# Performance work log

Hardware: AMD Instinct MI355X
Metric: run time of the kernel (lower is better)

Reference implementation:

```python
import jax, jax.numpy as jnp
import numpy as np

B, S, E, H, A, V, T = 64, 128, 512, 512, 256, 8192, 32


def setup_inputs() -> dict:
    key = jax.random.key(0)
    ks = jax.random.split(key, 10)
    sc = 0.02
    b_lstm = jnp.zeros((4 * H,), jnp.float32).at[H:2 * H].set(1.0)  # forget-gate bias = 1
    return {
        "encoder_features": jax.random.normal(ks[0], (B, S, E), jnp.float32),
        "target_sequence": jax.random.randint(ks[1], (B, T), 0, V),
        "emb": jax.random.uniform(ks[2], (V, H), jnp.float32, -0.1, 0.1),
        "W_enc": jax.random.normal(ks[3], (E, A), jnp.float32) * sc,
        "W_dec": jax.random.normal(ks[4], (H, A), jnp.float32) * sc,
        "b_att": jnp.zeros((A,), jnp.float32),
        "v_att": jax.random.normal(ks[5], (A,), jnp.float32) * sc,
        "W_ih": jax.random.normal(ks[6], (4 * H, H + E), jnp.float32) * sc,
        "W_hh": jax.random.normal(ks[7], (4 * H, H), jnp.float32) * sc,
        "b_ih": b_lstm,
        "b_hh": jnp.zeros((4 * H,), jnp.float32),
        "W_out": jax.random.normal(ks[8], (V, H + E), jnp.float32) * sc,
        "b_out": jnp.zeros((V,), jnp.float32),
    }


def reference(encoder_features, target_sequence, emb, W_enc, W_dec, b_att, v_att,
              W_ih, W_hh, b_ih, b_hh, W_out, b_out):
    b, t = target_sequence.shape
    # teacher forcing: first input token is 0, then shifted targets -> [T, B]
    tokens = jnp.concatenate(
        [jnp.zeros((b, 1), target_sequence.dtype), target_sequence[:, :-1]], axis=1).T
    # precompute encoder projection of Bahdanau attention: [B, S, A]
    enc_proj = jnp.einsum('bse,ea->bsa', encoder_features, W_enc)
    bias = b_ih + b_hh
    h0 = jnp.zeros((b, H), encoder_features.dtype)
    c0 = jnp.zeros((b, H), encoder_features.dtype)

    def step(carry, tok):
        h, c = carry
        x_emb = jnp.take(emb, tok, axis=0)                      # [B, H]
        # Bahdanau attention using previous decoder hidden state h
        e = jnp.tanh(enc_proj + (h @ W_dec + b_att)[:, None, :])  # [B, S, A]
        scores = jnp.einsum('bsa,a->bs', e, v_att)               # [B, S]
        w = jax.nn.softmax(scores, axis=-1)
        ctx = jnp.einsum('bs,bse->be', w, encoder_features)      # [B, E]
        x = jnp.concatenate([x_emb, ctx], axis=-1)               # [B, H+E]
        gates = x @ W_ih.T + h @ W_hh.T + bias                   # [B, 4H]
        i, f, g, o = jnp.split(gates, 4, axis=-1)
        c_new = jax.nn.sigmoid(f) * c + jax.nn.sigmoid(i) * jnp.tanh(g)
        h_new = jax.nn.sigmoid(o) * jnp.tanh(c_new)
        out = jnp.concatenate([h_new, ctx], axis=-1) @ W_out.T + b_out  # [B, V]
        return (h_new, c_new), out

    _, outs = jax.lax.scan(step, (h0, c0), tokens)
    return outs.transpose(1, 0, 2)  # [B, T, V]
```

## Files before the change

### kernel.cpp

```cpp
#include <hip/hip_runtime.h>
#include <math.h>

#define BB 64
#define SS 128
#define EE 512
#define HH 512
#define AA 256
#define VV 8192
#define TT 32

typedef __bf16 bf16x8 __attribute__((ext_vector_type(8)));
typedef __bf16 bf16x4 __attribute__((ext_vector_type(4)));
typedef float  f32x4  __attribute__((ext_vector_type(4)));

__device__ __forceinline__ bf16x8 cvt_v(float4 u, float4 v) {
    bf16x8 r;
    r[0] = (__bf16)u.x; r[1] = (__bf16)u.y; r[2] = (__bf16)u.z; r[3] = (__bf16)u.w;
    r[4] = (__bf16)v.x; r[5] = (__bf16)v.y; r[6] = (__bf16)v.z; r[7] = (__bf16)v.w;
    return r;
}

__device__ __forceinline__ float tanh_fast(float x) {
    x = fminf(15.f, fmaxf(-15.f, x));
    float e = __expf(2.f * x);
    return (e - 1.f) / (e + 1.f);
}
__device__ __forceinline__ float sigmoid_fast(float x) {
    return 1.f / (1.f + __expf(-x));
}

#define LDW(d, p) { const float4* q_ = (const float4*)(p); d##0 = q_[0]; d##1 = q_[1]; d##2 = q_[2]; d##3 = q_[3]; }

__global__ __launch_bounds__(256) void gemm_nn(
    const float* __restrict__ A, int lda,
    const float* __restrict__ B, int ldb,
    float* __restrict__ C, int ldc, int K)
{
    __shared__ float As[16][68];
    __shared__ float Bs[16][68];
    const int tid = threadIdx.x;
    const int m0 = blockIdx.x * 64, n0 = blockIdx.y * 64;
    const int row = tid >> 2, kq = (tid & 3) * 4;
    const int kk = tid >> 4, nq = (tid & 15) * 4;
    const int tm = tid >> 4, tn = tid & 15;
    float acc[4][4] = {};
    for (int k0 = 0; k0 < K; k0 += 16) {
        float4 av = *(const float4*)(A + (size_t)(m0 + row) * lda + k0 + kq);
        float4 bv = *(const float4*)(B + (size_t)(k0 + kk) * ldb + n0 + nq);
        As[kq + 0][row] = av.x; As[kq + 1][row] = av.y;
        As[kq + 2][row] = av.z; As[kq + 3][row] = av.w;
        *(float4*)&Bs[kk][nq] = bv;
        __syncthreads();
#pragma unroll
        for (int k = 0; k < 16; ++k) {
            float4 a = *(const float4*)&As[k][tm * 4];
            float4 b = *(const float4*)&Bs[k][tn * 4];
            acc[0][0] += a.x * b.x; acc[0][1] += a.x * b.y; acc[0][2] += a.x * b.z; acc[0][3] += a.x * b.w;
            acc[1][0] += a.y * b.x; acc[1][1] += a.y * b.y; acc[1][2] += a.y * b.z; acc[1][3] += a.y * b.w;
            acc[2][0] += a.z * b.x; acc[2][1] += a.z * b.y; acc[2][2] += a.z * b.z; acc[2][3] += a.z * b.w;
            acc[3][0] += a.w * b.x; acc[3][1] += a.w * b.y; acc[3][2] += a.w * b.z; acc[3][3] += a.w * b.w;
        }
        __syncthreads();
    }
#pragma unroll
    for (int i = 0; i < 4; ++i) {
        float4 r = make_float4(acc[i][0], acc[i][1], acc[i][2], acc[i][3]);
        *(float4*)(C + (size_t)(m0 + tm * 4 + i) * ldc + n0 + tn * 4) = r;
    }
}

__global__ __launch_bounds__(256) void k_cvt_bf16(
    const float* __restrict__ src, __bf16* __restrict__ dst, size_t n4)
{
    size_t i = (size_t)blockIdx.x * 256 + threadIdx.x;
    if (i < n4) {
        float4 v = *(const float4*)(src + i * 4);
        bf16x4 r;
        r[0] = (__bf16)v.x; r[1] = (__bf16)v.y; r[2] = (__bf16)v.z; r[3] = (__bf16)v.w;
        *(bf16x4*)(dst + i * 4) = r;
    }
}

__global__ __launch_bounds__(256) void k_cvt_gates(
    const float* __restrict__ W_ih, const float* __restrict__ W_hh,
    __bf16* __restrict__ Wg)
{
    const int n = blockIdx.x;
    const int j = ((n & 3) << 9) + (n >> 2);
    for (int k = threadIdx.x * 4; k < 1536; k += 1024) {
        const float* src = (k < 512)  ? (W_hh + (size_t)j * 512 + k)
                         : (k < 1024) ? (W_ih + (size_t)j * 1024 + k)
                                      : (W_ih + (size_t)j * 1024 + (k - 1024));
        float4 v = *(const float4*)src;
        bf16x4 r;
        r[0] = (__bf16)v.x; r[1] = (__bf16)v.y; r[2] = (__bf16)v.z; r[3] = (__bf16)v.w;
        *(bf16x4*)(Wg + (size_t)n * 1536 + k) = r;
    }
}

__global__ __launch_bounds__(1024) void attn_step(
    const float* __restrict__ encf,
    const float* __restrict__ encp,
    const float* __restrict__ W_dec,
    const float* __restrict__ b_att,
    const float* __restrict__ v_att,
    const float* __restrict__ emb,
    const int*   __restrict__ tgt,
    const float* __restrict__ h,
    __bf16* __restrict__ xh_cur,
    __bf16* __restrict__ XHN,
    int t)
{
    const int b = blockIdx.x;
    const int tid = threadIdx.x;
    __shared__ float sh[512];
    __shared__ float sdec[256];
    __shared__ float sv[256];
    __shared__ float sw[128], st[128];
    __shared__ float part[4][256];
    __shared__ float cpart[2][512];

    if (tid < 512) sh[tid] = h[(size_t)b * 512 + tid];
    else if (tid < 768) sv[tid - 512] = v_att[tid - 512];
    __syncthreads();

    {
        const int a = tid & 255, kq = tid >> 8;
        const float* w = W_dec + (size_t)kq * 128 * 256 + a;
        const float* hp = sh + kq * 128;
        float s = 0.f;
#pragma unroll 8
        for (int k = 0; k < 128; ++k) s += hp[k] * w[(size_t)k * 256];
        part[kq][a] = s;
    }
    __syncthreads();
    if (tid < 256)
        sdec[tid] = part[0][tid] + part[1][tid] + part[2][tid] + part[3][tid] + b_att[tid];
    __syncthreads();

    {
        const int wv = tid >> 6, lane = tid & 63;
#pragma unroll
        for (int i = 0; i < 8; ++i) {
            const int s = wv * 8 + i;
            const float* ep = encp + ((size_t)b * 128 + s) * 256;
            float sum = 0.f;
#pragma unroll
            for (int c = 0; c < 4; ++c) {
                int a = lane + 64 * c;
                sum += tanh_fast(ep[a] + sdec[a]) * sv[a];
            }
#pragma unroll
            for (int off = 32; off > 0; off >>= 1) sum += __shfl_down(sum, off);
            if (lane == 0) sw[s] = sum;
        }
    }
    __syncthreads();

    if (tid < 128) st[tid] = sw[tid];
    __syncthreads();
    for (int off = 64; off > 0; off >>= 1) {
        if (tid < off) st[tid] = fmaxf(st[tid], st[tid + off]);
        __syncthreads();
    }
    const float mx = st[0];
    __syncthreads();
    if (tid < 128) { float ex = __expf(sw[tid] - mx); sw[tid] = ex; st[tid] = ex; }
    __syncthreads();
    for (int off = 64; off > 0; off >>= 1) {
        if (tid < off) st[tid] += st[tid + off];
        __syncthreads();
    }

    {
        const int e = tid & 511, half = tid >> 9;
        const float* ef = encf + (size_t)b * (SS * EE) + (size_t)half * 64 * 512 + e;
        const float* wp = sw + half * 64;
        float cv = 0.f;
#pragma unroll 8
        for (int s = 0; s < 64; ++s) cv += wp[s] * ef[(size_t)s * 512];
        cpart[half][e] = cv;
    }
    __syncthreads();
    const float inv = 1.f / st[0];
    if (tid < 512) {
        const __bf16 cv = (__bf16)((cpart[0][tid] + cpart[1][tid]) * inv);
        xh_cur[(size_t)b * 1024 + tid] = cv;
        XHN[(size_t)(t * 64 + b) * 1024 + 512 + tid] = cv;
    } else {
        const int e = tid - 512;
        const int tok = (t == 0) ? 0 : tgt[b * TT + t - 1];
        xh_cur[(size_t)b * 1024 + 512 + e] = (__bf16)emb[(size_t)tok * 512 + e];
    }
}

template<bool BF16W>
__global__ __launch_bounds__(256) void gemm_gates_lstm(
    const __bf16* __restrict__ h_old,
    const __bf16* __restrict__ xh_ce,
    const float* __restrict__ W_ih, const float* __restrict__ W_hh,
    const __bf16* __restrict__ Wg,
    const float* __restrict__ b_ih, const float* __restrict__ b_hh,
    float* __restrict__ hbuf, float* __restrict__ cbuf,
    __bf16* __restrict__ h_new,
    __bf16* __restrict__ XHN, int t)
{
    __shared__ __align__(16) char smem[18432];
    __bf16 (*Ws)[32][72] = (__bf16 (*)[32][72])smem;
    float  (*Cf)[36]     = (float (*)[36])(smem + 9216);
    const int tid = threadIdx.x;
    const int wv = tid >> 6, lane = tid & 63;
    const int quad = lane >> 4, l16 = lane & 15;
    const int n0 = blockIdx.x * 32;
    const int rowW = tid >> 3, kq8 = (tid & 7) * 8;

    const __bf16* rB = nullptr;
    const float *rH = nullptr, *rI = nullptr;
    if constexpr (BF16W) {
        rB = Wg + (size_t)(n0 + rowW) * 1536 + kq8;
    } else {
        const int nglob = n0 + rowW;
        const int j = ((nglob & 3) << 9) + (nglob >> 2);
        rH = W_hh + (size_t)j * 512;
        rI = W_ih + (size_t)j * 1024;
    }
    auto wld = [&](int it) -> bf16x8 {
        if constexpr (BF16W) {
            return *(const bf16x8*)(rB + it * 64);
        } else {
            const int k = it * 64 + kq8;
            const float* s = (k < 512) ? (rH + k)
                           : (k < 1024 ? rI + k : rI + (k - 1024));
            const float4* q = (const float4*)s;
            return cvt_v(q[0], q[1]);
        }
    };
    const __bf16* aHp = h_old + (size_t)(wv * 16 + l16) * 512 + quad * 8;
    const __bf16* aXp = xh_ce + (size_t)(wv * 16 + l16) * 1024 + quad * 8;

    f32x4 acc[2] = {{0,0,0,0},{0,0,0,0}};
    bf16x8 wcur = wld(0), wnxt = wld(1);
    bf16x8 aC0 = *(const bf16x8*)aHp, aC1 = *(const bf16x8*)(aHp + 32);
    bf16x8 aN0, aN1;
    for (int it = 0; it < 24; ++it) {
        *(bf16x8*)&Ws[it & 1][rowW][kq8] = wcur;
        __syncthreads();
        wcur = wnxt;
        if (it + 2 < 24) wnxt = wld(it + 2);
        if (it + 1 < 24) {
            const int itn = it + 1;
            const __bf16* ap = (itn < 8) ? (aHp + itn * 64) : (aXp + (itn - 8) * 64);
            aN0 = *(const bf16x8*)ap; aN1 = *(const bf16x8*)(ap + 32);
        }
#pragma unroll
        for (int c = 0; c < 2; ++c) {
            bf16x8 b0 = *(const bf16x8*)&Ws[it & 1][c * 16 + l16][quad * 8];
            bf16x8 b1 = *(const bf16x8*)&Ws[it & 1][c * 16 + l16][quad * 8 + 32];
            acc[c] = __builtin_amdgcn_mfma_f32_16x16x32_bf16(aC0, b0, acc[c], 0, 0, 0);
            acc[c] = __builtin_amdgcn_mfma_f32_16x16x32_bf16(aC1, b1, acc[c], 0, 0, 0);
        }
        aC0 = aN0; aC1 = aN1;
    }
    __syncthreads();
#pragma unroll
    for (int r = 0; r < 4; ++r) {
        Cf[wv * 16 + quad * 4 + r][ 0 + l16] = acc[0][r];
        Cf[wv * 16 + quad * 4 + r][16 + l16] = acc[1][r];
    }
    __syncthreads();
    const int U0 = n0 >> 2;
#pragma unroll
    for (int pass = 0; pass < 2; ++pass) {
        const int it2 = tid + pass * 256;
        const int bb = it2 >> 3, ul = it2 & 7;
        const int u = U0 + ul;
        const float gi = Cf[bb][4 * ul + 0] + b_ih[u]          + b_hh[u];
        const float gf = Cf[bb][4 * ul + 1] + b_ih[512 + u]    + b_hh[512 + u];
        const float gg = Cf[bb][4 * ul + 2] + b_ih[1024 + u]   + b_hh[1024 + u];
        const float go = Cf[bb][4 * ul + 3] + b_ih[1536 + u]   + b_hh[1536 + u];
        const float si = sigmoid_fast(gi);
        const float sf = sigmoid_fast(gf);
        const float so = sigmoid_fast(go);
        const float cn = sf * cbuf[bb * 512 + u] + si * tanh_fast(gg);
        const float hn = so * tanh_fast(cn);
        cbuf[bb * 512 + u] = cn;
        hbuf[bb * 512 + u] = hn;
        const __bf16 hb = (__bf16)hn;
        h_new[(size_t)bb * 512 + u] = hb;
        if (XHN) XHN[(size_t)(t * 64 + bb) * 1024 + u] = hb;
    }
}

template<bool BF16W>
__global__ __launch_bounds__(256) void gemm_out_big(
    const __bf16* __restrict__ XHN,
    const float*  __restrict__ Wo_f,
    const __bf16* __restrict__ Wo_b,
    const float*  __restrict__ b_out,
    float* __restrict__ out)
{
    __shared__ __bf16 Bs[2][64][72];
    const int tid = threadIdx.x;
    const int blk = blockIdx.x;
    const int mt = blk & 15;
    const int n0 = (blk >> 4) * 64;
    const int wv = tid >> 6, lane = tid & 63;
    const int quad = lane >> 4, l16 = lane & 15;
    const int row = tid >> 2, cq = tid & 3;

    const __bf16* aP0 = XHN + (size_t)(mt * 128 + wv * 16 + l16) * 1024 + quad * 8;
    const __bf16* aP1 = aP0 + (size_t)64 * 1024;

    f32x4 acc[8] = {{0,0,0,0},{0,0,0,0},{0,0,0,0},{0,0,0,0},
                    {0,0,0,0},{0,0,0,0},{0,0,0,0},{0,0,0,0}};
    float4 wA0, wA1, wA2, wA3, wB0, wB1, wB2, wB3;
    bf16x8 pA0, pA1, pB0, pB1;
    const float*  bsf = nullptr;
    const __bf16* bsb = nullptr;
    if constexpr (BF16W) {
        bsb = Wo_b + (size_t)(n0 + row) * 1024 + cq * 16;
        const bf16x8* q0 = (const bf16x8*)bsb;        pA0 = q0[0]; pA1 = q0[1];
        const bf16x8* q1 = (const bf16x8*)(bsb + 64); pB0 = q1[0]; pB1 = q1[1];
    } else {
        bsf = Wo_f + (size_t)(n0 + row) * 1024 + cq * 16;
        LDW(wA, bsf); LDW(wB, bsf + 64);
    }
    bf16x8 a0C0 = *(const bf16x8*)aP0, a0C1 = *(const bf16x8*)(aP0 + 32);
    bf16x8 a1C0 = *(const bf16x8*)aP1, a1C1 = *(const bf16x8*)(aP1 + 32);
    bf16x8 a0N0, a0N1, a1N0, a1N1;

    for (int it = 0; it < 16; ++it) {
        __bf16* dst = &Bs[it & 1][row][cq * 16];
        if constexpr (BF16W) {
            *(bf16x8*)dst       = pA0;
            *(bf16x8*)(dst + 8) = pA1;
        } else {
            *(bf16x8*)dst       = cvt_v(wA0, wA1);
            *(bf16x8*)(dst + 8) = cvt_v(wA2, wA3);
        }
        __syncthreads();
        if constexpr (BF16W) {
            pA0 = pB0; pA1 = pB1;
            if (it + 2 < 16) {
                const bf16x8* q = (const bf16x8*)(bsb + (it + 2) * 64);
                pB0 = q[0]; pB1 = q[1];
            }
        } else {
            wA0 = wB0; wA1 = wB1; wA2 = wB2; wA3 = wB3;
            if (it + 2 < 16) LDW(wB, bsf + (it + 2) * 64);
        }
        if (it + 1 < 16) {
            const __bf16* ap0 = aP0 + (it + 1) * 64;
            const __bf16* ap1 = aP1 + (it + 1) * 64;
            a0N0 = *(const bf16x8*)ap0; a0N1 = *(const bf16x8*)(ap0 + 32);
            a1N0 = *(const bf16x8*)ap1; a1N1 = *(const bf16x8*)(ap1 + 32);
        }
#pragma unroll
        for (int c = 0; c < 4; ++c) {
            bf16x8 b0 = *(const bf16x8*)&Bs[it & 1][c * 16 + l16][quad * 8];
            bf16x8 b1 = *(const bf16x8*)&Bs[it & 1][c * 16 + l16][quad * 8 + 32];
            acc[c]     = __builtin_amdgcn_mfma_f32_16x16x32_bf16(a0C0, b0, acc[c],     0, 0, 0);
            acc[c]     = __builtin_amdgcn_mfma_f32_16x16x32_bf16(a0C1, b1, acc[c],     0, 0, 0);
            acc[4 + c] = __builtin_amdgcn_mfma_f32_16x16x32_bf16(a1C0, b0, acc[4 + c], 0, 0, 0);
            acc[4 + c] = __builtin_amdgcn_mfma_f32_16x16x32_bf16(a1C1, b1, acc[4 + c], 0, 0, 0);
        }
        a0C0 = a0N0; a0C1 = a0N1; a1C0 = a1N0; a1C1 = a1N1;
    }
    const int nb = n0 + l16;
#pragma unroll
    for (int h2 = 0; h2 < 2; ++h2) {
#pragma unroll
        for (int r = 0; r < 4; ++r) {
            const int rglob = mt * 128 + h2 * 64 + wv * 16 + quad * 4 + r;
            const int tstep = rglob >> 6, bb = rglob & 63;
            float* orow = out + (size_t)bb * (TT * VV) + (size_t)tstep * VV + nb;
            orow[ 0] = acc[h2 * 4 + 0][r] + b_out[nb +  0];
            orow[16] = acc[h2 * 4 + 1][r] + b_out[nb + 16];
            orow[32] = acc[h2 * 4 + 2][r] + b_out[nb + 32];
            orow[48] = acc[h2 * 4 + 3][r] + b_out[nb + 48];
        }
    }
}

template<bool BF16W>
__global__ __launch_bounds__(256) void fused_out_attn(
    const __bf16* __restrict__ hA, const __bf16* __restrict__ xA,
    const float*  __restrict__ Wo_f, const __bf16* __restrict__ Wo_b,
    const float*  __restrict__ b_out, float* __restrict__ out, int tprev,
    const float* __restrict__ encf, const float* __restrict__ encp,
    const float* __restrict__ W_dec, const float* __restrict__ b_att,
    const float* __restrict__ v_att, const float* __restrict__ emb,
    const int*   __restrict__ tgt, const float* __restrict__ h,
    __bf16* __restrict__ xh_cur, int t, int nOut)
{
    __shared__ __align__(16) char smem[18432];
    const int blk = blockIdx.x;
    const int tid = threadIdx.x;
    const int wv = tid >> 6, lane = tid & 63;
    const int quad = lane >> 4, l16 = lane & 15;

    if (blk < nOut) {
        __bf16 (*Bs)[64][72] = (__bf16 (*)[64][72])smem;
        const int n0 = blk * 64;
        const int row = tid >> 2, cq = tid & 3;
        const __bf16* aHp = hA + (size_t)(wv * 16 + l16) * 512 + quad * 8;
        const __bf16* aXp = xA + (size_t)(wv * 16 + l16) * 1024 + quad * 8;

        f32x4 acc[4] = {{0,0,0,0},{0,0,0,0},{0,0,0,0},{0,0,0,0}};
        bf16x8 aC0 = *(const bf16x8*)aHp, aC1 = *(const bf16x8*)(aHp + 32);
        bf16x8 aN0, aN1;
        float4 wA0, wA1, wA2, wA3, wB0, wB1, wB2, wB3;
        bf16x8 pA0, pA1, pB0, pB1;
        const float*  bsf = nullptr;
        const __bf16* bsb = nullptr;
        if constexpr (BF16W) {
            bsb = Wo_b + (size_t)(n0 + row) * 1024 + cq * 16;
            const bf16x8* q0 = (const bf16x8*)bsb;        pA0 = q0[0]; pA1 = q0[1];
            const bf16x8* q1 = (const bf16x8*)(bsb + 64); pB0 = q1[0]; pB1 = q1[1];
        } else {
            bsf = Wo_f + (size_t)(n0 + row) * 1024 + cq * 16;
            LDW(wA, bsf); LDW(wB, bsf + 64);
        }
        for (int it = 0; it < 16; ++it) {
            __bf16* dst = &Bs[it & 1][row][cq * 16];
            if constexpr (BF16W) {
                *(bf16x8*)dst       = pA0;
                *(bf16x8*)(dst + 8) = pA1;
            } else {
                *(bf16x8*)dst       = cvt_v(wA0, wA1);
                *(bf16x8*)(dst + 8) = cvt_v(wA2, wA3);
            }
            __syncthreads();
            if constexpr (BF16W) {
                pA0 = pB0; pA1 = pB1;
                if (it + 2 < 16) {
                    const bf16x8* q = (const bf16x8*)(bsb + (it + 2) * 64);
                    pB0 = q[0]; pB1 = q[1];
                }
            } else {
                wA0 = wB0; wA1 = wB1; wA2 = wB2; wA3 = wB3;
                if (it + 2 < 16) LDW(wB, bsf + (it + 2) * 64);
            }
            if (it + 1 < 16) {
                const int itn = it + 1;
                const __bf16* ap = (itn < 8) ? (aHp + itn * 64) : (aXp + (itn - 8) * 64);
                aN0 = *(const bf16x8*)ap; aN1 = *(const bf16x8*)(ap + 32);
            }
#pragma unroll
            for (int c = 0; c < 4; ++c) {
                bf16x8 b0 = *(const bf16x8*)&Bs[it & 1][c * 16 + l16][quad * 8];
                bf16x8 b1 = *(const bf16x8*)&Bs[it & 1][c * 16 + l16][quad * 8 + 32];
                acc[c] = __builtin_amdgcn_mfma_f32_16x16x32_bf16(aC0, b0, acc[c], 0, 0, 0);
                acc[c] = __builtin_amdgcn_mfma_f32_16x16x32_bf16(aC1, b1, acc[c], 0, 0, 0);
            }
            aC0 = aN0; aC1 = aN1;
        }
        const int m = wv * 16 + quad * 4;
        const int nb = n0 + l16;
        float* op = out + (size_t)tprev * VV + nb;
#pragma unroll
        for (int r = 0; r < 4; ++r) {
            float* orow = op + (size_t)(m + r) * (TT * VV);
            orow[ 0] = acc[0][r] + b_out[nb +  0];
            orow[16] = acc[1][r] + b_out[nb + 16];
            orow[32] = acc[2][r] + b_out[nb + 32];
            orow[48] = acc[3][r] + b_out[nb + 48];
        }
    } else {
        const int b = blk - nOut;
        float* sh   = (float*)smem;
        float* sdec = sh + 512;
        float* sv   = sdec + 256;
        float* sw   = sv + 256;
        sh[tid] = h[(size_t)b * 512 + tid];
        sh[tid + 256] = h[(size_t)b * 512 + 256 + tid];
        sv[tid] = v_att[tid];
        __syncthreads();
        {
            const float* w = W_dec + tid;
            float s = 0.f;
#pragma unroll 8
            for (int k = 0; k < 512; ++k) s += sh[k] * w[(size_t)k * 256];
            sdec[tid] = s + b_att[tid];
        }
        __syncthreads();
        {
            const float* ep0 = encp + ((size_t)b * 128 + wv * 32) * 256;
            for (int i = 0; i < 32; ++i) {
                const float* ep = ep0 + (size_t)i * 256;
                float sum = 0.f;
#pragma unroll
                for (int c = 0; c < 4; ++c) {
                    int a = lane + 64 * c;
                    sum += tanh_fast(ep[a] + sdec[a]) * sv[a];
                }
#pragma unroll
                for (int off = 32; off > 0; off >>= 1) sum += __shfl_down(sum, off);
                if (lane == 0) sw[wv * 32 + i] = sum;
            }
        }
        __syncthreads();
        if (tid < 64) {
            float a0 = sw[tid], a1 = sw[tid + 64];
            float m = fmaxf(a0, a1);
#pragma unroll
            for (int off = 32; off > 0; off >>= 1) m = fmaxf(m, __shfl_xor(m, off));
            float e0 = __expf(a0 - m), e1 = __expf(a1 - m);
            sw[tid] = e0; sw[tid + 64] = e1;
            float ss = e0 + e1;
#pragma unroll
            for (int off = 32; off > 0; off >>= 1) ss += __shfl_xor(ss, off);
            if (tid == 0) sh[0] = ss;
        }
        __syncthreads();
        const float inv = 1.f / sh[0];
        {
            const float* ef = encf + (size_t)b * (SS * EE) + tid;
            float cv0 = 0.f, cv1 = 0.f;
#pragma unroll 8
            for (int s = 0; s < 128; ++s) {
                float w = sw[s];
                cv0 += w * ef[(size_t)s * 512];
                cv1 += w * ef[(size_t)s * 512 + 256];
            }
            xh_cur[(size_t)b * 1024 + tid]       = (__bf16)(cv0 * inv);
            xh_cur[(size_t)b * 1024 + 256 + tid] = (__bf16)(cv1 * inv);
        }
        {
            const int tok = (t == 0) ? 0 : tgt[b * TT + t - 1];
            const float* em = emb + (size_t)tok * 512;
            xh_cur[(size_t)b * 1024 + 512 + tid] = (__bf16)em[tid];
            xh_cur[(size_t)b * 1024 + 768 + tid] = (__bf16)em[tid + 256];
        }
    }
}

__global__ void k_zero_f(float* p, int n) {
    int i = blockIdx.x * 256 + threadIdx.x;
    if (i < n) p[i] = 0.f;
}
__global__ void k_zero_bf(__bf16* p, int n) {
    int i = blockIdx.x * 256 + threadIdx.x;
    if (i < n) p[i] = (__bf16)0.f;
}

extern "C" void kernel_launch(void* const* d_in, const int* in_sizes, int n_in,
                              void* d_out, int out_size, void* d_ws, size_t ws_size,
                              hipStream_t stream)
{
    (void)in_sizes; (void)n_in; (void)out_size;
    const float* encf  = (const float*)d_in[0];
    const int*   tgt   = (const int*)  d_in[1];
    const float* emb   = (const float*)d_in[2];
    const float* W_enc = (const float*)d_in[3];
    const float* W_dec = (const float*)d_in[4];
    const float* b_att = (const float*)d_in[5];
    const float* v_att = (const float*)d_in[6];
    const float* W_ih  = (const float*)d_in[7];
    const float* W_hh  = (const float*)d_in[8];
    const float* b_ih  = (const float*)d_in[9];
    const float* b_hh  = (const float*)d_in[10];
    const float* W_out = (const float*)d_in[11];
    const float* b_out = (const float*)d_in[12];
    float* out = (float*)d_out;

    float* ws = (float*)d_ws;
    size_t off = 0;
    auto alloc = [&](size_t n) { float* p = ws + off; off += (n + 255) & ~(size_t)255; return p; };
    float*  encp = alloc((size_t)BB * SS * AA);
    float*  hbuf = alloc((size_t)BB * HH);
    float*  cbuf = alloc((size_t)BB * HH);
    __bf16* xh0  = (__bf16*)alloc((size_t)BB * 1024 / 2);
    __bf16* xh1  = (__bf16*)alloc((size_t)BB * 1024 / 2);
    __bf16* hb0  = (__bf16*)alloc((size_t)BB * HH / 2);
    __bf16* hb1  = (__bf16*)alloc((size_t)BB * HH / 2);
    __bf16* XHN  = (__bf16*)alloc((size_t)2048 * 1024 / 2);
    __bf16* Wg   = (__bf16*)alloc((size_t)2048 * 1536 / 2);
    const size_t off1 = off;
    __bf16* Wo_b = (__bf16*)alloc((size_t)VV * 1024 / 2);
    const size_t off2 = off;

    const int level = (off2 * sizeof(float) <= ws_size) ? 2
                    : (off1 * sizeof(float) <= ws_size) ? 1 : 0;

    k_zero_f<<<(2 * BB * HH + 255) / 256, 256, 0, stream>>>(hbuf, 2 * BB * HH);
    k_zero_bf<<<(BB * HH + 255) / 256, 256, 0, stream>>>(hb0, BB * HH);
    gemm_nn<<<dim3(BB * SS / 64, AA / 64), 256, 0, stream>>>(encf, EE, W_enc, AA, encp, AA, EE);

    if (level >= 1) {
        k_cvt_gates<<<2048, 256, 0, stream>>>(W_ih, W_hh, Wg);
        if (level == 2)
            k_cvt_bf16<<<(int)(((size_t)VV * 1024 / 4 + 255) / 256), 256, 0, stream>>>(
                W_out, Wo_b, (size_t)VV * 1024 / 4);

        for (int t = 0; t < TT; ++t) {
            __bf16* hold = (t & 1) ? hb1 : hb0;
            __bf16* hnew = (t & 1) ? hb0 : hb1;
            attn_step<<<64, 1024, 0, stream>>>(
                encf, encp, W_dec, b_att, v_att, emb, tgt, hbuf, xh0, XHN, t);
            gemm_gates_lstm<true><<<64, 256, 0, stream>>>(
                hold, xh0, W_ih, W_hh, Wg, b_ih, b_hh, hbuf, cbuf, hnew, XHN, t);
        }
        if (level == 2)
            gemm_out_big<true><<<2048, 256, 0, stream>>>(XHN, W_out, Wo_b, b_out, out);
        else
            gemm_out_big<false><<<2048, 256, 0, stream>>>(XHN, W_out, Wo_b, b_out, out);
    } else {
        fused_out_attn<false><<<64, 256, 0, stream>>>(
            hb0, xh0, W_out, Wo_b, b_out, out, 0,
            encf, encp, W_dec, b_att, v_att, emb, tgt, hbuf, xh0, 0, 0);
        gemm_gates_lstm<false><<<64, 256, 0, stream>>>(
            hb0, xh0, W_ih, W_hh, Wg, b_ih, b_hh, hbuf, cbuf, hb1, nullptr, 0);
        for (int t = 1; t < TT; ++t) {
            __bf16* hold = (t & 1) ? hb1 : hb0;
            __bf16* hnew = (t & 1) ? hb0 : hb1;
            __bf16* xhp  = ((t - 1) & 1) ? xh1 : xh0;
            __bf16* xhc  = (t & 1) ? xh1 : xh0;
            fused_out_attn<false><<<192, 256, 0, stream>>>(
                hold, xhp, W_out, Wo_b, b_out, out, t - 1,
                encf, encp, W_dec, b_att, v_att, emb, tgt, hbuf, xhc, t, 128);
            gemm_gates_lstm<false><<<64, 256, 0, stream>>>(
                hold, xhc, W_ih, W_hh, Wg, b_ih, b_hh, hbuf, cbuf, hnew, nullptr, 0);
        }
        fused_out_attn<false><<<128, 256, 0, stream>>>(
            hb0, xh1, W_out, Wo_b, b_out, out, TT - 1,
            encf, encp, W_dec, b_att, v_att, emb, tgt, hbuf, xh0, 0, 128);
    }
}
```

Baseline: 1.174 ms.

## Fuse recurrent attention and LSTM steps into one persistent cooperative kernel

```diff
diff --git a/kernel.cpp b/kernel.cpp
--- a/kernel.cpp
+++ b/kernel.cpp
@@ -30,6 +30,27 @@
 }
 
 #define LDW(d, p) { const float4* q_ = (const float4*)(p); d##0 = q_[0]; d##1 = q_[1]; d##2 = q_[2]; d##3 = q_[3]; }
+
+__device__ __forceinline__ void gbar(int* bar, int nblk) {
+    __syncthreads();
+    if (threadIdx.x == 0) {
+        __threadfence();
+        int g = __hip_atomic_load(&bar[1], __ATOMIC_RELAXED, __HIP_MEMORY_SCOPE_AGENT);
+        int a = __hip_atomic_fetch_add(&bar[0], 1, __ATOMIC_ACQ_REL, __HIP_MEMORY_SCOPE_AGENT);
+        if (a == nblk - 1) {
+            __hip_atomic_store(&bar[0], 0, __ATOMIC_RELAXED, __HIP_MEMORY_SCOPE_AGENT);
+            __hip_atomic_fetch_add(&bar[1], 1, __ATOMIC_RELEASE, __HIP_MEMORY_SCOPE_AGENT);
+        } else {
+            int spins = 0;
+            while (__hip_atomic_load(&bar[1], __ATOMIC_ACQUIRE, __HIP_MEMORY_SCOPE_AGENT) == g) {
+                __builtin_amdgcn_s_sleep(2);
+                if (++spins > (1 << 27)) break;
+            }
+        }
+        __threadfence();
+    }
+    __syncthreads();
+}
 
 __global__ __launch_bounds__(256) void gemm_nn(
     const float* __restrict__ A, int lda,
@@ -98,18 +119,172 @@
     }
 }
 
+struct PB {
+    const float* encf; const float* encp; const float* W_dec; const float* b_att;
+    const float* v_att; const float* emb; const int* tgt;
+    const __bf16* Wg; const float* b_ih; const float* b_hh;
+    float* hbuf; float* cbuf;
+    __bf16* xh; __bf16* hb0; __bf16* hb1; __bf16* XHN;
+    int* bar;
+};
+
+__global__ __launch_bounds__(256) void persist2(PB p)
+{
+    __shared__ __align__(16) char smem[18432];
+    const int blk = blockIdx.x;
+    const int tid = threadIdx.x;
+    const int wv = tid >> 6, lane = tid & 63;
+    const int quad = lane >> 4, l16 = lane & 15;
+
+    for (int t = 0; t < TT; ++t) {
+        const __bf16* hold = (t & 1) ? p.hb1 : p.hb0;
+        __bf16* hnew = (t & 1) ? p.hb0 : p.hb1;
+
+        {
+            const int b = blk;
+            float* sh   = (float*)smem;
+            float* sdec = sh + 512;
+            float* sv   = sdec + 256;
+            float* sw   = sv + 256;
+            sh[tid] = p.hbuf[(size_t)b * 512 + tid];
+            sh[tid + 256] = p.hbuf[(size_t)b * 512 + 256 + tid];
+            sv[tid] = p.v_att[tid];
+            __syncthreads();
+            {
+                const float* w = p.W_dec + tid;
+                float s = 0.f;
+#pragma unroll 8
+                for (int k = 0; k < 512; ++k) s += sh[k] * w[(size_t)k * 256];
+                sdec[tid] = s + p.b_att[tid];
+            }
+            __syncthreads();
+            {
+                const float* ep0 = p.encp + ((size_t)b * 128 + wv * 32) * 256;
+                for (int i = 0; i < 32; ++i) {
+                    const float* ep = ep0 + (size_t)i * 256;
+                    float sum = 0.f;
+#pragma unroll
+                    for (int c = 0; c < 4; ++c) {
+                        int a = lane + 64 * c;
+                        sum += tanh_fast(ep[a] + sdec[a]) * sv[a];
+                    }
+#pragma unroll
+                    for (int off = 32; off > 0; off >>= 1) sum += __shfl_down(sum, off);
+                    if (lane == 0) sw[wv * 32 + i] = sum;
+                }
+            }
+            __syncthreads();
+            if (tid < 64) {
+                float a0 = sw[tid], a1 = sw[tid + 64];
+                float m = fmaxf(a0, a1);
+#pragma unroll
+                for (int off = 32; off > 0; off >>= 1) m = fmaxf(m, __shfl_xor(m, off));
+                float e0 = __expf(a0 - m), e1 = __expf(a1 - m);
+                sw[tid] = e0; sw[tid + 64] = e1;
+                float ss = e0 + e1;
+#pragma unroll
+                for (int off = 32; off > 0; off >>= 1) ss += __shfl_xor(ss, off);
+                if (tid == 0) sh[0] = ss;
+            }
+            __syncthreads();
+            const float inv = 1.f / sh[0];
+            {
+                const float* ef = p.encf + (size_t)b * (SS * EE) + tid;
+                float cv0 = 0.f, cv1 = 0.f;
+#pragma unroll 8
+                for (int s = 0; s < 128; ++s) {
+                    float w = sw[s];
+                    cv0 += w * ef[(size_t)s * 512];
+                    cv1 += w * ef[(size_t)s * 512 + 256];
+                }
+                const __bf16 c0 = (__bf16)(cv0 * inv);
+                const __bf16 c1 = (__bf16)(cv1 * inv);
+                p.xh[(size_t)b * 1024 + tid]       = c0;
+                p.xh[(size_t)b * 1024 + 256 + tid] = c1;
+                p.XHN[(size_t)(t * 64 + b) * 1024 + 512 + tid]       = c0;
+                p.XHN[(size_t)(t * 64 + b) * 1024 + 768 + tid]       = c1;
+            }
+            {
+                const int tok = (t == 0) ? 0 : p.tgt[b * TT + t - 1];
+                const float* em = p.emb + (size_t)tok * 512;
+                p.xh[(size_t)b * 1024 + 512 + tid] = (__bf16)em[tid];
+                p.xh[(size_t)b * 1024 + 768 + tid] = (__bf16)em[tid + 256];
+            }
+        }
+        gbar(p.bar, 64);
+
+        {
+            __bf16 (*Ws)[32][72] = (__bf16 (*)[32][72])smem;
+            float  (*Cf)[36]     = (float (*)[36])(smem + 9216);
+            const int n0 = blk * 32;
+            const int rowW = tid >> 3, kq8 = (tid & 7) * 8;
+            const __bf16* rB = p.Wg + (size_t)(n0 + rowW) * 1536 + kq8;
+            const __bf16* aHp = hold + (size_t)(wv * 16 + l16) * 512 + quad * 8;
+            const __bf16* aXp = p.xh + (size_t)(wv * 16 + l16) * 1024 + quad * 8;
+
+            f32x4 acc[2] = {{0,0,0,0},{0,0,0,0}};
+            bf16x8 wcur = *(const bf16x8*)rB;
+            bf16x8 wnxt = *(const bf16x8*)(rB + 64);
+            bf16x8 aC0 = *(const bf16x8*)aHp, aC1 = *(const bf16x8*)(aHp + 32);
+            bf16x8 aN0, aN1;
+            for (int it = 0; it < 24; ++it) {
+                *(bf16x8*)&Ws[it & 1][rowW][kq8] = wcur;
+                __syncthreads();
+                wcur = wnxt;
+                if (it + 2 < 24) wnxt = *(const bf16x8*)(rB + (it + 2) * 64);
+                if (it + 1 < 24) {
+                    const int itn = it + 1;
+                    const __bf16* ap = (itn < 8) ? (aHp + itn * 64) : (aXp + (itn - 8) * 64);
+                    aN0 = *(const bf16x8*)ap; aN1 = *(const bf16x8*)(ap + 32);
+                }
+#pragma unroll
+                for (int c = 0; c < 2; ++c) {
+                    bf16x8 b0 = *(const bf16x8*)&Ws[it & 1][c * 16 + l16][quad * 8];
+                    bf16x8 b1 = *(const bf16x8*)&Ws[it & 1][c * 16 + l16][quad * 8 + 32];
+                    acc[c] = __builtin_amdgcn_mfma_f32_16x16x32_bf16(aC0, b0, acc[c], 0, 0, 0);
+                    acc[c] = __builtin_amdgcn_mfma_f32_16x16x32_bf16(aC1, b1, acc[c], 0, 0, 0);
+                }
+                aC0 = aN0; aC1 = aN1;
+            }
+            __syncthreads();
+#pragma unroll
+            for (int r = 0; r < 4; ++r) {
+                Cf[wv * 16 + quad * 4 + r][ 0 + l16] = acc[0][r];
+                Cf[wv * 16 + quad * 4 + r][16 + l16] = acc[1][r];
+            }
+            __syncthreads();
+            const int U0 = n0 >> 2;
+#pragma unroll
+            for (int pass = 0; pass < 2; ++pass) {
+                const int it2 = tid + pass * 256;
+                const int bb = it2 >> 3, ul = it2 & 7;
+                const int u = U0 + ul;
+                const float gi = Cf[bb][4 * ul + 0] + p.b_ih[u]          + p.b_hh[u];
+                const float gf = Cf[bb][4 * ul + 1] + p.b_ih[512 + u]    + p.b_hh[512 + u];
+                const float gg = Cf[bb][4 * ul + 2] + p.b_ih[1024 + u]   + p.b_hh[1024 + u];
+                const float go = Cf[bb][4 * ul + 3] + p.b_ih[1536 + u]   + p.b_hh[1536 + u];
+                const float si = sigmoid_fast(gi);
+                const float sf = sigmoid_fast(gf);
+                const float so = sigmoid_fast(go);
+                const float cn = sf * p.cbuf[bb * 512 + u] + si * tanh_fast(gg);
+                const float hn = so * tanh_fast(cn);
+                p.cbuf[bb * 512 + u] = cn;
+                p.hbuf[bb * 512 + u] = hn;
+                const __bf16 hb = (__bf16)hn;
+                hnew[(size_t)bb * 512 + u] = hb;
+                p.XHN[(size_t)(t * 64 + bb) * 1024 + u] = hb;
+            }
+        }
+        gbar(p.bar, 64);
+    }
+}
+
 __global__ __launch_bounds__(1024) void attn_step(
-    const float* __restrict__ encf,
-    const float* __restrict__ encp,
-    const float* __restrict__ W_dec,
-    const float* __restrict__ b_att,
-    const float* __restrict__ v_att,
-    const float* __restrict__ emb,
-    const int*   __restrict__ tgt,
-    const float* __restrict__ h,
-    __bf16* __restrict__ xh_cur,
-    __bf16* __restrict__ XHN,
-    int t)
+    const float* __restrict__ encf, const float* __restrict__ encp,
+    const float* __restrict__ W_dec, const float* __restrict__ b_att,
+    const float* __restrict__ v_att, const float* __restrict__ emb,
+    const int*   __restrict__ tgt, const float* __restrict__ h,
+    __bf16* __restrict__ xh_cur, __bf16* __restrict__ XHN, int t)
 {
     const int b = blockIdx.x;
     const int tid = threadIdx.x;
@@ -123,7 +298,6 @@
     if (tid < 512) sh[tid] = h[(size_t)b * 512 + tid];
     else if (tid < 768) sv[tid - 512] = v_att[tid - 512];
     __syncthreads();
-
     {
         const int a = tid & 255, kq = tid >> 8;
         const float* w = W_dec + (size_t)kq * 128 * 256 + a;
@@ -137,7 +311,6 @@
     if (tid < 256)
         sdec[tid] = part[0][tid] + part[1][tid] + part[2][tid] + part[3][tid] + b_att[tid];
     __syncthreads();
-
     {
         const int wv = tid >> 6, lane = tid & 63;
 #pragma unroll
@@ -156,7 +329,6 @@
         }
     }
     __syncthreads();
-
     if (tid < 128) st[tid] = sw[tid];
     __syncthreads();
     for (int off = 64; off > 0; off >>= 1) {
@@ -171,7 +343,6 @@
         if (tid < off) st[tid] += st[tid + off];
         __syncthreads();
     }
-
     {
         const int e = tid & 511, half = tid >> 9;
         const float* ef = encf + (size_t)b * (SS * EE) + (size_t)half * 64 * 512 + e;
@@ -196,14 +367,12 @@
 
 template<bool BF16W>
 __global__ __launch_bounds__(256) void gemm_gates_lstm(
-    const __bf16* __restrict__ h_old,
-    const __bf16* __restrict__ xh_ce,
+    const __bf16* __restrict__ h_old, const __bf16* __restrict__ xh_ce,
     const float* __restrict__ W_ih, const float* __restrict__ W_hh,
     const __bf16* __restrict__ Wg,
     const float* __restrict__ b_ih, const float* __restrict__ b_hh,
     float* __restrict__ hbuf, float* __restrict__ cbuf,
-    __bf16* __restrict__ h_new,
-    __bf16* __restrict__ XHN, int t)
+    __bf16* __restrict__ h_new, __bf16* __restrict__ XHN, int t)
 {
     __shared__ __align__(16) char smem[18432];
     __bf16 (*Ws)[32][72] = (__bf16 (*)[32][72])smem;
@@ -299,11 +468,11 @@
     const float*  __restrict__ b_out,
     float* __restrict__ out)
 {
-    __shared__ __bf16 Bs[2][64][72];
+    __shared__ __bf16 Bs[2][64][76];
     const int tid = threadIdx.x;
-    const int blk = blockIdx.x;
-    const int mt = blk & 15;
-    const int n0 = (blk >> 4) * 64;
+    const int blks = ((blockIdx.x & 7) << 8) | ((int)blockIdx.x >> 3);
+    const int mt = blks & 15;
+    const int n0 = (blks >> 4) * 64;
     const int wv = tid >> 6, lane = tid & 63;
     const int quad = lane >> 4, l16 = lane & 15;
     const int row = tid >> 2, cq = tid & 3;
@@ -378,159 +547,6 @@
             orow[16] = acc[h2 * 4 + 1][r] + b_out[nb + 16];
             orow[32] = acc[h2 * 4 + 2][r] + b_out[nb + 32];
             orow[48] = acc[h2 * 4 + 3][r] + b_out[nb + 48];
-        }
-    }
-}
-
-template<bool BF16W>
-__global__ __launch_bounds__(256) void fused_out_attn(
-    const __bf16* __restrict__ hA, const __bf16* __restrict__ xA,
-    const float*  __restrict__ Wo_f, const __bf16* __restrict__ Wo_b,
-    const float*  __restrict__ b_out, float* __restrict__ out, int tprev,
-    const float* __restrict__ encf, const float* __restrict__ encp,
-    const float* __restrict__ W_dec, const float* __restrict__ b_att,
-    const float* __restrict__ v_att, const float* __restrict__ emb,
-    const int*   __restrict__ tgt, const float* __restrict__ h,
-    __bf16* __restrict__ xh_cur, int t, int nOut)
-{
-    __shared__ __align__(16) char smem[18432];
-    const int blk = blockIdx.x;
-    const int tid = threadIdx.x;
-    const int wv = tid >> 6, lane = tid & 63;
-    const int quad = lane >> 4, l16 = lane & 15;
-
-    if (blk < nOut) {
-        __bf16 (*Bs)[64][72] = (__bf16 (*)[64][72])smem;
-        const int n0 = blk * 64;
-        const int row = tid >> 2, cq = tid & 3;
-        const __bf16* aHp = hA + (size_t)(wv * 16 + l16) * 512 + quad * 8;
-        const __bf16* aXp = xA + (size_t)(wv * 16 + l16) * 1024 + quad * 8;
-
-        f32x4 acc[4] = {{0,0,0,0},{0,0,0,0},{0,0,0,0},{0,0,0,0}};
-        bf16x8 aC0 = *(const bf16x8*)aHp, aC1 = *(const bf16x8*)(aHp + 32);
-        bf16x8 aN0, aN1;
-        float4 wA0, wA1, wA2, wA3, wB0, wB1, wB2, wB3;
-        bf16x8 pA0, pA1, pB0, pB1;
-        const float*  bsf = nullptr;
-        const __bf16* bsb = nullptr;
-        if constexpr (BF16W) {
-            bsb = Wo_b + (size_t)(n0 + row) * 1024 + cq * 16;
-            const bf16x8* q0 = (const bf16x8*)bsb;        pA0 = q0[0]; pA1 = q0[1];
-            const bf16x8* q1 = (const bf16x8*)(bsb + 64); pB0 = q1[0]; pB1 = q1[1];
-        } else {
-            bsf = Wo_f + (size_t)(n0 + row) * 1024 + cq * 16;
-            LDW(wA, bsf); LDW(wB, bsf + 64);
-        }
-        for (int it = 0; it < 16; ++it) {
-            __bf16* dst = &Bs[it & 1][row][cq * 16];
-            if constexpr (BF16W) {
-                *(bf16x8*)dst       = pA0;
-                *(bf16x8*)(dst + 8) = pA1;
-            } else {
-                *(bf16x8*)dst       = cvt_v(wA0, wA1);
-                *(bf16x8*)(dst + 8) = cvt_v(wA2, wA3);
-            }
-            __syncthreads();
-            if constexpr (BF16W) {
-                pA0 = pB0; pA1 = pB1;
-                if (it + 2 < 16) {
-                    const bf16x8* q = (const bf16x8*)(bsb + (it + 2) * 64);
-                    pB0 = q[0]; pB1 = q[1];
-                }
-            } else {
-                wA0 = wB0; wA1 = wB1; wA2 = wB2; wA3 = wB3;
-                if (it + 2 < 16) LDW(wB, bsf + (it + 2) * 64);
-            }
-            if (it + 1 < 16) {
-                const int itn = it + 1;
-                const __bf16* ap = (itn < 8) ? (aHp + itn * 64) : (aXp + (itn - 8) * 64);
-                aN0 = *(const bf16x8*)ap; aN1 = *(const bf16x8*)(ap + 32);
-            }
-#pragma unroll
-            for (int c = 0; c < 4; ++c) {
-                bf16x8 b0 = *(const bf16x8*)&Bs[it & 1][c * 16 + l16][quad * 8];
-                bf16x8 b1 = *(const bf16x8*)&Bs[it & 1][c * 16 + l16][quad * 8 + 32];
-                acc[c] = __builtin_amdgcn_mfma_f32_16x16x32_bf16(aC0, b0, acc[c], 0, 0, 0);
-                acc[c] = __builtin_amdgcn_mfma_f32_16x16x32_bf16(aC1, b1, acc[c], 0, 0, 0);
-            }
-            aC0 = aN0; aC1 = aN1;
-        }
-        const int m = wv * 16 + quad * 4;
-        const int nb = n0 + l16;
-        float* op = out + (size_t)tprev * VV + nb;
-#pragma unroll
-        for (int r = 0; r < 4; ++r) {
-            float* orow = op + (size_t)(m + r) * (TT * VV);
-            orow[ 0] = acc[0][r] + b_out[nb +  0];
-            orow[16] = acc[1][r] + b_out[nb + 16];
-            orow[32] = acc[2][r] + b_out[nb + 32];
-            orow[48] = acc[3][r] + b_out[nb + 48];
-        }
-    } else {
-        const int b = blk - nOut;
-        float* sh   = (float*)smem;
-        float* sdec = sh + 512;
-        float* sv   = sdec + 256;
-        float* sw   = sv + 256;
-        sh[tid] = h[(size_t)b * 512 + tid];
-        sh[tid + 256] = h[(size_t)b * 512 + 256 + tid];
-        sv[tid] = v_att[tid];
-        __syncthreads();
-        {
-            const float* w = W_dec + tid;
-            float s = 0.f;
-#pragma unroll 8
-            for (int k = 0; k < 512; ++k) s += sh[k] * w[(size_t)k * 256];
-            sdec[tid] = s + b_att[tid];
-        }
-        __syncthreads();
-        {
-            const float* ep0 = encp + ((size_t)b * 128 + wv * 32) * 256;
-            for (int i = 0; i < 32; ++i) {
-                const float* ep = ep0 + (size_t)i * 256;
-                float sum = 0.f;
-#pragma unroll
-                for (int c = 0; c < 4; ++c) {
-                    int a = lane + 64 * c;
-                    sum += tanh_fast(ep[a] + sdec[a]) * sv[a];
-                }
-#pragma unroll
-                for (int off = 32; off > 0; off >>= 1) sum += __shfl_down(sum, off);
-                if (lane == 0) sw[wv * 32 + i] = sum;
-            }
-        }
-        __syncthreads();
-        if (tid < 64) {
-            float a0 = sw[tid], a1 = sw[tid + 64];
-            float m = fmaxf(a0, a1);
-#pragma unroll
-            for (int off = 32; off > 0; off >>= 1) m = fmaxf(m, __shfl_xor(m, off));
-            float e0 = __expf(a0 - m), e1 = __expf(a1 - m);
-            sw[tid] = e0; sw[tid + 64] = e1;
-            float ss = e0 + e1;
-#pragma unroll
-            for (int off = 32; off > 0; off >>= 1) ss += __shfl_xor(ss, off);
-            if (tid == 0) sh[0] = ss;
-        }
-        __syncthreads();
-        const float inv = 1.f / sh[0];
-        {
-            const float* ef = encf + (size_t)b * (SS * EE) + tid;
-            float cv0 = 0.f, cv1 = 0.f;
-#pragma unroll 8
-            for (int s = 0; s < 128; ++s) {
-                float w = sw[s];
-                cv0 += w * ef[(size_t)s * 512];
-                cv1 += w * ef[(size_t)s * 512 + 256];
-            }
-            xh_cur[(size_t)b * 1024 + tid]       = (__bf16)(cv0 * inv);
-            xh_cur[(size_t)b * 1024 + 256 + tid] = (__bf16)(cv1 * inv);
-        }
-        {
-            const int tok = (t == 0) ? 0 : tgt[b * TT + t - 1];
-            const float* em = emb + (size_t)tok * 512;
-            xh_cur[(size_t)b * 1024 + 512 + tid] = (__bf16)em[tid];
-            xh_cur[(size_t)b * 1024 + 768 + tid] = (__bf16)em[tid + 256];
         }
     }
 }
@@ -570,6 +586,7 @@
     float*  encp = alloc((size_t)BB * SS * AA);
     float*  hbuf = alloc((size_t)BB * HH);
     float*  cbuf = alloc((size_t)BB * HH);
+    int*    bar  = (int*)alloc(256);
     __bf16* xh0  = (__bf16*)alloc((size_t)BB * 1024 / 2);
     __bf16* xh1  = (__bf16*)alloc((size_t)BB * 1024 / 2);
     __bf16* hb0  = (__bf16*)alloc((size_t)BB * HH / 2);
@@ -583,7 +600,7 @@
     const int level = (off2 * sizeof(float) <= ws_size) ? 2
                     : (off1 * sizeof(float) <= ws_size) ? 1 : 0;
 
-    k_zero_f<<<(2 * BB * HH + 255) / 256, 256, 0, stream>>>(hbuf, 2 * BB * HH);
+    k_zero_f<<<(2 * BB * HH + 256 + 255) / 256, 256, 0, stream>>>(hbuf, 2 * BB * HH + 256);
     k_zero_bf<<<(BB * HH + 255) / 256, 256, 0, stream>>>(hb0, BB * HH);
     gemm_nn<<<dim3(BB * SS / 64, AA / 64), 256, 0, stream>>>(encf, EE, W_enc, AA, encp, AA, EE);
 
@@ -593,37 +610,40 @@
             k_cvt_bf16<<<(int)(((size_t)VV * 1024 / 4 + 255) / 256), 256, 0, stream>>>(
                 W_out, Wo_b, (size_t)VV * 1024 / 4);
 
+        PB pb;
+        pb.encf = encf; pb.encp = encp; pb.W_dec = W_dec; pb.b_att = b_att;
+        pb.v_att = v_att; pb.emb = emb; pb.tgt = tgt;
+        pb.Wg = Wg; pb.b_ih = b_ih; pb.b_hh = b_hh;
+        pb.hbuf = hbuf; pb.cbuf = cbuf;
+        pb.xh = xh0; pb.hb0 = hb0; pb.hb1 = hb1; pb.XHN = XHN;
+        pb.bar = bar;
+        void* kargs[] = { &pb };
+        void (*fp)(PB) = persist2;
+        hipError_t rc = hipLaunchCooperativeKernel((const void*)fp, dim3(64), dim3(256),
+                                                   kargs, 0, stream);
+        if (rc != hipSuccess) {
+            for (int t = 0; t < TT; ++t) {
+                __bf16* hold = (t & 1) ? hb1 : hb0;
+                __bf16* hnew = (t & 1) ? hb0 : hb1;
+                attn_step<<<64, 1024, 0, stream>>>(
+                    encf, encp, W_dec, b_att, v_att, emb, tgt, hbuf, xh0, XHN, t);
+                gemm_gates_lstm<true><<<64, 256, 0, stream>>>(
+                    hold, xh0, W_ih, W_hh, Wg, b_ih, b_hh, hbuf, cbuf, hnew, XHN, t);
+            }
+        }
+        if (level == 2)
+            gemm_out_big<true><<<2048, 256, 0, stream>>>(XHN, W_out, Wo_b, b_out, out);
+        else
+            gemm_out_big<false><<<2048, 256, 0, stream>>>(XHN, W_out, Wo_b, b_out, out);
+    } else {
         for (int t = 0; t < TT; ++t) {
             __bf16* hold = (t & 1) ? hb1 : hb0;
             __bf16* hnew = (t & 1) ? hb0 : hb1;
             attn_step<<<64, 1024, 0, stream>>>(
                 encf, encp, W_dec, b_att, v_att, emb, tgt, hbuf, xh0, XHN, t);
-            gemm_gates_lstm<true><<<64, 256, 0, stream>>>(
-                hold, xh0, W_ih, W_hh, Wg, b_ih, b_hh, hbuf, cbuf, hnew, XHN, t);
-        }
-        if (level == 2)
-            gemm_out_big<true><<<2048, 256, 0, stream>>>(XHN, W_out, Wo_b, b_out, out);
-        else
-            gemm_out_big<false><<<2048, 256, 0, stream>>>(XHN, W_out, Wo_b, b_out, out);
-    } else {
-        fused_out_attn<false><<<64, 256, 0, stream>>>(
-            hb0, xh0, W_out, Wo_b, b_out, out, 0,
-            encf, encp, W_dec, b_att, v_att, emb, tgt, hbuf, xh0, 0, 0);
-        gemm_gates_lstm<false><<<64, 256, 0, stream>>>(
-            hb0, xh0, W_ih, W_hh, Wg, b_ih, b_hh, hbuf, cbuf, hb1, nullptr, 0);
-        for (int t = 1; t < TT; ++t) {
-            __bf16* hold = (t & 1) ? hb1 : hb0;
-            __bf16* hnew = (t & 1) ? hb0 : hb1;
-            __bf16* xhp  = ((t - 1) & 1) ? xh1 : xh0;
-            __bf16* xhc  = (t & 1) ? xh1 : xh0;
-            fused_out_attn<false><<<192, 256, 0, stream>>>(
-                hold, xhp, W_out, Wo_b, b_out, out, t - 1,
-                encf, encp, W_dec, b_att, v_att, emb, tgt, hbuf, xhc, t, 128);
             gemm_gates_lstm<false><<<64, 256, 0, stream>>>(
-                hold, xhc, W_ih, W_hh, Wg, b_ih, b_hh, hbuf, cbuf, hnew, nullptr, 0);
-        }
-        fused_out_attn<false><<<128, 256, 0, stream>>>(
-            hb0, xh1, W_out, Wo_b, b_out, out, TT - 1,
-            encf, encp, W_dec, b_att, v_att, emb, tgt, hbuf, xh0, 0, 128);
-    }
-}
+                hold, xh0, W_ih, W_hh, nullptr, b_ih, b_hh, hbuf, cbuf, hnew, XHN, t);
+        }
+        gemm_out_big<false><<<2048, 256, 0, stream>>>(XHN, W_out, nullptr, b_out, out);
+    }
+}
```

Measured after the change: 2.508 ms. 2.14x slower.
